# Kernel tuning notes

Measured on AMD Instinct MI355X. Metric: run time of the kernel, lower is better.

Reference implementation:

```python
import jax, jax.numpy as jnp
import numpy as np
from jax import lax

V, D, H, C = 32000, 300, 300, 3
B, T = 128, 512


def setup_inputs() -> dict:
    key = jax.random.key(0)
    ks = jax.random.split(key, 8)
    sentence_ids = jax.random.randint(ks[0], (B, T), 0, V, dtype=jnp.int32)
    lengths = jnp.maximum(jax.random.randint(ks[1], (B,), 0, T, dtype=jnp.int32), 1)
    labels = jax.random.randint(ks[2], (B,), 0, C, dtype=jnp.int32)
    embedding = jax.random.normal(ks[3], (V, D), jnp.float32) * 0.1
    W_lstm = jax.random.normal(ks[4], (D + H, 4 * H), jnp.float32) * 0.05
    b_lstm = jnp.zeros((4 * H,), jnp.float32)
    W_dense = jax.random.normal(ks[5], (H, C), jnp.float32) * 0.05
    b_dense = jnp.zeros((C,), jnp.float32)
    return {"sentence_ids": sentence_ids, "lengths": lengths, "labels": labels,
            "embedding": embedding, "W_lstm": W_lstm, "b_lstm": b_lstm,
            "W_dense": W_dense, "b_dense": b_dense}


def reference(sentence_ids, lengths, labels, embedding, W_lstm, b_lstm, W_dense, b_dense):
    # Embedding lookup: [B, T, D]
    x = embedding[sentence_ids]
    b, t, d = x.shape
    h_units = W_dense.shape[0]
    FORGET_BIAS = 1.0  # TF BasicLSTMCell default

    xs = jnp.swapaxes(x, 0, 1)                                   # [T, B, D]
    step_mask = (jnp.arange(t)[:, None] < lengths[None, :])      # [T, B]

    def step(carry, inp):
        h, c = carry
        xt, m = inp                                              # [B,D], [B]
        z = jnp.concatenate([xt, h], axis=-1) @ W_lstm + b_lstm  # [B, 4H]
        i, j, f, o = jnp.split(z, 4, axis=-1)
        new_c = c * jax.nn.sigmoid(f + FORGET_BIAS) + jax.nn.sigmoid(i) * jnp.tanh(j)
        new_h = jnp.tanh(new_c) * jax.nn.sigmoid(o)
        mm = m[:, None]
        # dynamic_rnn: freeze state past each sequence's length
        h = jnp.where(mm, new_h, h)
        c = jnp.where(mm, new_c, c)
        return (h, c), None

    h0 = jnp.zeros((b, h_units), x.dtype)
    c0 = jnp.zeros((b, h_units), x.dtype)
    (h_final, _), _ = lax.scan(step, (h0, c0), (xs, step_mask))

    logits = h_final @ W_dense + b_dense                          # [B, C]
    logp = jax.nn.log_softmax(logits, axis=-1)
    nll = -jnp.take_along_axis(logp, labels[:, None].astype(jnp.int32), axis=1)[:, 0]
    loss = jnp.mean(nll)
    return loss, logits
```

## Files before the change

kernel.cpp:

```cpp
#include <hip/hip_runtime.h>
#include <hip/hip_bf16.h>
#include <math.h>

#define VV   32000
#define DD   300
#define HU   300
#define NC   3
#define BB   128
#define TT   512
#define N4H  1200
#define CHUNK 64
#define NCHUNK (TT / CHUNK)

#define GC   15
#define GR   16
#define RPW  8
#define UPW  20
#define KSW  96
#define HLB_STRIDE 312
#define HLB_SIZE   (16 * HLB_STRIDE + 32)

static constexpr size_t ZX_F   = (size_t)BB * CHUNK * N4H;
static constexpr size_t EX_W   = (size_t)2 * GR * RPW * HU;
static constexpr size_t CST_F  = (size_t)BB * HU;
static constexpr size_t HFIN_F = (size_t)BB * HU;

typedef __attribute__((ext_vector_type(8))) short bf16x8;
typedef __attribute__((ext_vector_type(8))) _Float16 f16x8;
typedef __attribute__((ext_vector_type(4))) float f32x4;
typedef unsigned long long ull;

__device__ __forceinline__ short f2bf(float f) {
    unsigned u = __float_as_uint(f);
    u += 0x7fff + ((u >> 16) & 1);
    return (short)(u >> 16);
}
__device__ __forceinline__ short f2h(float f) {
    _Float16 h = (_Float16)f;
    return *(short*)&h;
}
__device__ __forceinline__ float h2f(short s) {
    _Float16 h = *(_Float16*)&s;
    return (float)h;
}
__device__ __forceinline__ float sigm(float x) { return 1.f / (1.f + __expf(-x)); }
__device__ __forceinline__ float tanh_(float x) { return 1.f - 2.f / (__expf(2.f * x) + 1.f); }

__global__ void init_kernel(ull* __restrict__ ex, float* __restrict__ cst,
                            float* __restrict__ out) {
    size_t i = (size_t)blockIdx.x * 256 + threadIdx.x;
    if (i < EX_W) ex[i] = 0ull;
    if (i < CST_F) cst[i] = 0.f;
    if (i == 0) out[0] = 0.f;
}

__global__ __launch_bounds__(256) void zx_gemm(
    const float* __restrict__ emb, const int* __restrict__ ids,
    const float* __restrict__ Wl, const float* __restrict__ bl,
    float* __restrict__ zx, int t0)
{
    __shared__ short A_l[256 * 40];
    __shared__ short B_l[80 * 40];
    __shared__ int   ids_l[256];

    const int tid = threadIdx.x;
    const int m0  = blockIdx.x * 256;
    const int n0  = blockIdx.y * 80;
    const int wv  = tid >> 6, ln = tid & 63;

    {
        int m = m0 + tid;
        int b = m >> 6, tc = m & (CHUNK - 1);
        ids_l[tid] = ids[b * TT + t0 + tc];
    }

    f32x4 acc[4][5];
    for (int i = 0; i < 4; ++i)
        for (int j = 0; j < 5; ++j)
            acc[i][j] = (f32x4){0.f, 0.f, 0.f, 0.f};

    for (int k0 = 0; k0 < 320; k0 += 32) {
        __syncthreads();
        {
            const float* src = emb + (size_t)ids_l[tid] * DD;
            #pragma unroll
            for (int q = 0; q < 8; ++q) {
                int kg = k0 + q * 4;
                float4 v;
                if (kg < DD) v = *(const float4*)(src + kg);
                else         v = make_float4(0.f, 0.f, 0.f, 0.f);
                short4 s; s.x = f2bf(v.x); s.y = f2bf(v.y); s.z = f2bf(v.z); s.w = f2bf(v.w);
                *(short4*)&A_l[tid * 40 + q * 4] = s;
            }
        }
        {
            int kk = tid >> 3;
            int c0 = (tid & 7) * 10;
            int kg = k0 + kk;
            #pragma unroll
            for (int c = 0; c < 10; ++c) {
                float v = (kg < DD) ? Wl[(size_t)kg * N4H + n0 + c0 + c] : 0.f;
                B_l[(c0 + c) * 40 + kk] = f2bf(v);
            }
        }
        __syncthreads();
        const int koff = (ln >> 4) * 8;
        bf16x8 afr[4], bfr[5];
        #pragma unroll
        for (int mt = 0; mt < 4; ++mt) {
            int row = wv * 64 + mt * 16 + (ln & 15);
            afr[mt] = *(const bf16x8*)&A_l[row * 40 + koff];
        }
        #pragma unroll
        for (int nt = 0; nt < 5; ++nt) {
            int col = nt * 16 + (ln & 15);
            bfr[nt] = *(const bf16x8*)&B_l[col * 40 + koff];
        }
        #pragma unroll
        for (int mt = 0; mt < 4; ++mt)
            #pragma unroll
            for (int nt = 0; nt < 5; ++nt)
                acc[mt][nt] = __builtin_amdgcn_mfma_f32_16x16x32_bf16(
                    afr[mt], bfr[nt], acc[mt][nt], 0, 0, 0);
    }
    #pragma unroll
    for (int mt = 0; mt < 4; ++mt) {
        #pragma unroll
        for (int nt = 0; nt < 5; ++nt) {
            #pragma unroll
            for (int rg = 0; rg < 4; ++rg) {
                int row = m0 + wv * 64 + mt * 16 + (ln >> 4) * 4 + rg;
                int col = n0 + nt * 16 + (ln & 15);
                zx[(size_t)row * N4H + col] = acc[mt][nt][rg] + bl[col];
            }
        }
    }
}

__global__ __launch_bounds__(256, 1) void lstm_rec(
    const float* __restrict__ zx, const float* __restrict__ Wl,
    const int* __restrict__ lens, ull* __restrict__ ex,
    float* __restrict__ cst, float* __restrict__ hfin, int t0)
{
    const int tid = threadIdx.x;
    const int wv  = tid >> 6, ln = tid & 63;
    const int rg  = blockIdx.x % GR;
    const int cgi = blockIdx.x / GR;
    const int r0  = rg * RPW;
    const int u0  = cgi * UPW;
    const int m   = ln & 15;
    const int quad = ln >> 4;

    const int pstart_tbl[4] = {0, 4, 9, 14};
    const int np_tbl[4]     = {5, 6, 6, 1};
    const int pstart = pstart_tbl[wv];
    const int np     = np_tbl[wv];

    __shared__ short h_hi[HLB_SIZE];
    __shared__ short h_lo[HLB_SIZE];
    __shared__ float zp[2][4][RPW][84];
    __shared__ short w_l[4 * 15 * 64 * 8];

    #pragma unroll
    for (int s = 0; s < 3; ++s) {
        #pragma unroll
        for (int nt = 0; nt < 5; ++nt) {
            int c    = nt * 16 + m;
            int gate = c / 20;
            int wcol = 300 * gate + u0 + (c % 20);
            f16x8 b;
            #pragma unroll
            for (int j = 0; j < 8; ++j) {
                int k = KSW * wv + 32 * s + quad * 8 + j;
                float v = (k < HU) ? Wl[(size_t)(DD + k) * N4H + wcol] : 0.f;
                b[j] = (_Float16)v;
            }
            *(f16x8*)&w_l[(((wv * 15) + (s * 5 + nt)) * 64 + ln) * 8] = b;
        }
    }
    const int nks = (wv == 3) ? 1 : 3;

    for (int i = tid; i < HLB_SIZE; i += 256) { h_hi[i] = 0; h_lo[i] = 0; }

    const int g_u = tid % UPW, g_r = tid / UPW;
    const bool gl = (tid < RPW * UPW);
    float c_reg = 0.f, ho_reg = 0.f;
    int mylen = 0;
    if (gl) {
        c_reg = cst[(size_t)(r0 + g_r) * HU + u0 + g_u];
        mylen = lens[r0 + g_r];
        if (t0 > 0) {
            ull v = __hip_atomic_load(
                ex + (((size_t)(t0 & 1) * GR + rg) * RPW + g_r) * HU + u0 + g_u,
                __ATOMIC_RELAXED, __HIP_MEMORY_SCOPE_AGENT);
            ho_reg = __uint_as_float((unsigned)v);
        }
    }
    __syncthreads();

    for (int tc = 0; tc < CHUNK; ++tc) {
        const int t = t0 + tc;
        const int par = t & 1;

        float z_pre[4];
        if (gl) {
            const float* zrow = zx + ((size_t)(r0 + g_r) * CHUNK + tc) * N4H;
            #pragma unroll
            for (int gg = 0; gg < 4; ++gg)
                z_pre[gg] = zrow[300 * gg + u0 + g_u];
        }

        if (t > 0) {
            const ull* exb = ex + ((size_t)par * GR + rg) * (RPW * HU);

            if (ln < np) {
                const ull* sp = exb + (pstart + ln) * UPW;
                while ((int)(__hip_atomic_load(sp, __ATOMIC_RELAXED,
                             __HIP_MEMORY_SCOPE_AGENT) >> 32) < t)
                    __builtin_amdgcn_s_sleep(1);
            }

            if (wv < 3) {
                unsigned pend = 0xFFFu;
                do {
                    ull v[12];
                    #pragma unroll
                    for (int k = 0; k < 12; ++k)
                        if ((pend >> k) & 1) {
                            int i = ln + (k << 6);
                            int r = i / 96, u = KSW * wv + (i % 96);
                            v[k] = __hip_atomic_load(exb + r * HU + u,
                                                     __ATOMIC_RELAXED,
                                                     __HIP_MEMORY_SCOPE_AGENT);
                        }
                    unsigned got = 0;
                    #pragma unroll
                    for (int k = 0; k < 12; ++k) {
                        if (((pend >> k) & 1) && (int)(v[k] >> 32) >= t) {
                            int i = ln + (k << 6);
                            int r = i / 96, u = KSW * wv + (i % 96);
                            int idx = r * HLB_STRIDE + u;
                            float f = __uint_as_float((unsigned)v[k]);
                            short hi = f2h(f);
                            h_hi[idx] = hi;
                            h_lo[idx] = f2h(f - h2f(hi));
                            got |= 1u << k;
                        }
                    }
                    pend &= ~got;
                    if (pend) __builtin_amdgcn_s_sleep(1);
                } while (pend);
            } else {
                unsigned pend = (ln < 32) ? 0x3u : 0x1u;
                do {
                    ull v[2];
                    #pragma unroll
                    for (int k = 0; k < 2; ++k)
                        if ((pend >> k) & 1) {
                            int i = ln + (k << 6);
                            int r = i / 12, u = 288 + (i % 12);
                            v[k] = __hip_atomic_load(exb + r * HU + u,
                                                     __ATOMIC_RELAXED,
                                                     __HIP_MEMORY_SCOPE_AGENT);
                        }
                    unsigned got = 0;
                    #pragma unroll
                    for (int k = 0; k < 2; ++k) {
                        if (((pend >> k) & 1) && (int)(v[k] >> 32) >= t) {
                            int i = ln + (k << 6);
                            int r = i / 12, u = 288 + (i % 12);
                            int idx = r * HLB_STRIDE + u;
                            float f = __uint_as_float((unsigned)v[k]);
                            short hi = f2h(f);
                            h_hi[idx] = hi;
                            h_lo[idx] = f2h(f - h2f(hi));
                            got |= 1u << k;
                        }
                    }
                    pend &= ~got;
                    if (pend) __builtin_amdgcn_s_sleep(1);
                } while (pend);
            }
        }

        f32x4 acc[5];
        #pragma unroll
        for (int nt = 0; nt < 5; ++nt) acc[nt] = (f32x4){0.f, 0.f, 0.f, 0.f};
        for (int s = 0; s < nks; ++s) {
            const int aoff = m * HLB_STRIDE + KSW * wv + 32 * s + quad * 8;
            f16x8 ah = *(const f16x8*)&h_hi[aoff];
            f16x8 al = *(const f16x8*)&h_lo[aoff];
            f16x8 bfr[5];
            #pragma unroll
            for (int nt = 0; nt < 5; ++nt)
                bfr[nt] = *(const f16x8*)&w_l[(((wv * 15) + (s * 5 + nt)) * 64 + ln) * 8];
            #pragma unroll
            for (int nt = 0; nt < 5; ++nt)
                acc[nt] = __builtin_amdgcn_mfma_f32_16x16x32_f16(
                    ah, bfr[nt], acc[nt], 0, 0, 0);
            #pragma unroll
            for (int nt = 0; nt < 5; ++nt)
                acc[nt] = __builtin_amdgcn_mfma_f32_16x16x32_f16(
                    al, bfr[nt], acc[nt], 0, 0, 0);
        }
        if (ln < 32) {
            #pragma unroll
            for (int nt = 0; nt < 5; ++nt)
                #pragma unroll
                for (int r4 = 0; r4 < 4; ++r4)
                    zp[par][wv][quad * 4 + r4][nt * 16 + m] = acc[nt][r4];
        }
        __syncthreads();

        if (gl) {
            const int b = r0 + g_r;
            float z4[4];
            #pragma unroll
            for (int gg = 0; gg < 4; ++gg) {
                int cidx = gg * UPW + g_u;
                z4[gg] = z_pre[gg] + zp[par][0][g_r][cidx] + zp[par][1][g_r][cidx]
                                   + zp[par][2][g_r][cidx] + zp[par][3][g_r][cidx];
            }
            float ig = sigm(z4[0]);
            float jg = tanh_(z4[1]);
            float fg = sigm(z4[2] + 1.0f);
            float og = sigm(z4[3]);
            float c_new = c_reg * fg + ig * jg;
            float h_new = tanh_(c_new) * og;
            bool upd = (t < mylen);
            ho_reg = upd ? h_new : ho_reg;
            c_reg  = upd ? c_new : c_reg;
            ull pk = ((ull)(unsigned)(t + 1) << 32) | (ull)__float_as_uint(ho_reg);
            __hip_atomic_store(
                ex + (((size_t)((t + 1) & 1) * GR + rg) * RPW + g_r) * HU + u0 + g_u,
                pk, __ATOMIC_RELAXED, __HIP_MEMORY_SCOPE_AGENT);
            if (tc == CHUNK - 1) hfin[(size_t)b * HU + u0 + g_u] = ho_reg;
        }
    }
    if (gl) cst[(size_t)(r0 + g_r) * HU + u0 + g_u] = c_reg;
}

__global__ __launch_bounds__(64) void cls_kernel(
    const float* __restrict__ hfin, const float* __restrict__ Wd,
    const float* __restrict__ bd, const int* __restrict__ labels,
    float* __restrict__ out)
{
    const int b = blockIdx.x;
    const int ln = threadIdx.x;
    const float* h = hfin + (size_t)b * HU;
    float p0 = 0.f, p1 = 0.f, p2 = 0.f;
    for (int k = ln; k < HU; k += 64) {
        float hv = h[k];
        p0 += hv * Wd[k * 3 + 0];
        p1 += hv * Wd[k * 3 + 1];
        p2 += hv * Wd[k * 3 + 2];
    }
    #pragma unroll
    for (int off = 32; off > 0; off >>= 1) {
        p0 += __shfl_down(p0, off);
        p1 += __shfl_down(p1, off);
        p2 += __shfl_down(p2, off);
    }
    if (ln == 0) {
        float l0 = p0 + bd[0], l1 = p1 + bd[1], l2 = p2 + bd[2];
        float m = fmaxf(l0, fmaxf(l1, l2));
        float lse = m + logf(__expf(l0 - m) + __expf(l1 - m) + __expf(l2 - m));
        int lab = labels[b];
        float sel = (lab == 0) ? l0 : ((lab == 1) ? l1 : l2);
        float nll = lse - sel;
        out[1 + b * 3 + 0] = l0;
        out[1 + b * 3 + 1] = l1;
        out[1 + b * 3 + 2] = l2;
        atomicAdd(out, nll * (1.0f / BB));
    }
}

extern "C" void kernel_launch(void* const* d_in, const int* in_sizes, int n_in,
                              void* d_out, int out_size, void* d_ws, size_t ws_size,
                              hipStream_t stream) {
    const int*   ids  = (const int*)d_in[0];
    const int*   lens = (const int*)d_in[1];
    const int*   labs = (const int*)d_in[2];
    const float* emb  = (const float*)d_in[3];
    const float* Wl   = (const float*)d_in[4];
    const float* bl   = (const float*)d_in[5];
    const float* Wd   = (const float*)d_in[6];
    const float* bd   = (const float*)d_in[7];
    float* out = (float*)d_out;

    float* zx   = (float*)d_ws;
    ull*   ex   = (ull*)(zx + ZX_F);
    float* cst  = (float*)(ex + EX_W);
    float* hfin = cst + CST_F;

    {
        int n = (int)((EX_W + 255) / 256);
        init_kernel<<<n, 256, 0, stream>>>(ex, cst, out);
    }
    for (int c = 0; c < NCHUNK; ++c) {
        int t0 = c * CHUNK;
        zx_gemm<<<dim3(32, 15), 256, 0, stream>>>(emb, ids, Wl, bl, zx, t0);
        lstm_rec<<<GR * GC, 256, 0, stream>>>(zx, Wl, lens, ex, cst, hfin, t0);
    }
    cls_kernel<<<BB, 64, 0, stream>>>(hfin, Wd, bd, labs, out);
}
```

Before: 2.312 ms.

## Fuse input projection GEMM into recurrent LSTM kernel per timestep

Removes the separate zx_gemm kernel and its global zx buffer. Inside the recurrent kernel each wave now gathers the embedding rows for its batch rows at each timestep, converts them to bf16, and runs an extra bf16 MFMA against an input-weight slice kept in shared memory, adding the result into the same accumulator as the hidden-state product. The intent is to drop the global write and read of the precomputed gate inputs and the per-chunk kernel launches. In exchange every step adds embedding gather latency and more MFMAs to the serial critical path, and the double-buffered zp array is replaced by a single buffer guarded by an extra barrier per step.

```diff
diff --git a/kernel.cpp b/kernel.cpp
--- a/kernel.cpp
+++ b/kernel.cpp
@@ -20,7 +20,6 @@
 #define HLB_STRIDE 312
 #define HLB_SIZE   (16 * HLB_STRIDE + 32)
 
-static constexpr size_t ZX_F   = (size_t)BB * CHUNK * N4H;
 static constexpr size_t EX_W   = (size_t)2 * GR * RPW * HU;
 static constexpr size_t CST_F  = (size_t)BB * HU;
 static constexpr size_t HFIN_F = (size_t)BB * HU;
@@ -54,91 +53,9 @@
     if (i == 0) out[0] = 0.f;
 }
 
-__global__ __launch_bounds__(256) void zx_gemm(
+__global__ __launch_bounds__(256, 1) void lstm_rec(
     const float* __restrict__ emb, const int* __restrict__ ids,
     const float* __restrict__ Wl, const float* __restrict__ bl,
-    float* __restrict__ zx, int t0)
-{
-    __shared__ short A_l[256 * 40];
-    __shared__ short B_l[80 * 40];
-    __shared__ int   ids_l[256];
-
-    const int tid = threadIdx.x;
-    const int m0  = blockIdx.x * 256;
-    const int n0  = blockIdx.y * 80;
-    const int wv  = tid >> 6, ln = tid & 63;
-
-    {
-        int m = m0 + tid;
-        int b = m >> 6, tc = m & (CHUNK - 1);
-        ids_l[tid] = ids[b * TT + t0 + tc];
-    }
-
-    f32x4 acc[4][5];
-    for (int i = 0; i < 4; ++i)
-        for (int j = 0; j < 5; ++j)
-            acc[i][j] = (f32x4){0.f, 0.f, 0.f, 0.f};
-
-    for (int k0 = 0; k0 < 320; k0 += 32) {
-        __syncthreads();
-        {
-            const float* src = emb + (size_t)ids_l[tid] * DD;
-            #pragma unroll
-            for (int q = 0; q < 8; ++q) {
-                int kg = k0 + q * 4;
-                float4 v;
-                if (kg < DD) v = *(const float4*)(src + kg);
-                else         v = make_float4(0.f, 0.f, 0.f, 0.f);
-                short4 s; s.x = f2bf(v.x); s.y = f2bf(v.y); s.z = f2bf(v.z); s.w = f2bf(v.w);
-                *(short4*)&A_l[tid * 40 + q * 4] = s;
-            }
-        }
-        {
-            int kk = tid >> 3;
-            int c0 = (tid & 7) * 10;
-            int kg = k0 + kk;
-            #pragma unroll
-            for (int c = 0; c < 10; ++c) {
-                float v = (kg < DD) ? Wl[(size_t)kg * N4H + n0 + c0 + c] : 0.f;
-                B_l[(c0 + c) * 40 + kk] = f2bf(v);
-            }
-        }
-        __syncthreads();
-        const int koff = (ln >> 4) * 8;
-        bf16x8 afr[4], bfr[5];
-        #pragma unroll
-        for (int mt = 0; mt < 4; ++mt) {
-            int row = wv * 64 + mt * 16 + (ln & 15);
-            afr[mt] = *(const bf16x8*)&A_l[row * 40 + koff];
-        }
-        #pragma unroll
-        for (int nt = 0; nt < 5; ++nt) {
-            int col = nt * 16 + (ln & 15);
-            bfr[nt] = *(const bf16x8*)&B_l[col * 40 + koff];
-        }
-        #pragma unroll
-        for (int mt = 0; mt < 4; ++mt)
-            #pragma unroll
-            for (int nt = 0; nt < 5; ++nt)
-                acc[mt][nt] = __builtin_amdgcn_mfma_f32_16x16x32_bf16(
-                    afr[mt], bfr[nt], acc[mt][nt], 0, 0, 0);
-    }
-    #pragma unroll
-    for (int mt = 0; mt < 4; ++mt) {
-        #pragma unroll
-        for (int nt = 0; nt < 5; ++nt) {
-            #pragma unroll
-            for (int rg = 0; rg < 4; ++rg) {
-                int row = m0 + wv * 64 + mt * 16 + (ln >> 4) * 4 + rg;
-                int col = n0 + nt * 16 + (ln & 15);
-                zx[(size_t)row * N4H + col] = acc[mt][nt][rg] + bl[col];
-            }
-        }
-    }
-}
-
-__global__ __launch_bounds__(256, 1) void lstm_rec(
-    const float* __restrict__ zx, const float* __restrict__ Wl,
     const int* __restrict__ lens, ull* __restrict__ ex,
     float* __restrict__ cst, float* __restrict__ hfin, int t0)
 {
@@ -158,8 +75,10 @@
 
     __shared__ short h_hi[HLB_SIZE];
     __shared__ short h_lo[HLB_SIZE];
-    __shared__ float zp[2][4][RPW][84];
+    __shared__ float zp[4][RPW][84];
     __shared__ short w_l[4 * 15 * 64 * 8];
+    __shared__ short w_lx[4 * 15 * 64 * 8];
+    __shared__ int   ids_l[RPW][CHUNK];
 
     #pragma unroll
     for (int s = 0; s < 3; ++s) {
@@ -168,27 +87,40 @@
             int c    = nt * 16 + m;
             int gate = c / 20;
             int wcol = 300 * gate + u0 + (c % 20);
-            f16x8 b;
+            f16x8 bh;
+            bf16x8 bx;
             #pragma unroll
             for (int j = 0; j < 8; ++j) {
                 int k = KSW * wv + 32 * s + quad * 8 + j;
-                float v = (k < HU) ? Wl[(size_t)(DD + k) * N4H + wcol] : 0.f;
-                b[j] = (_Float16)v;
-            }
-            *(f16x8*)&w_l[(((wv * 15) + (s * 5 + nt)) * 64 + ln) * 8] = b;
+                float vh = (k < HU) ? Wl[(size_t)(DD + k) * N4H + wcol] : 0.f;
+                float vx = (k < DD) ? Wl[(size_t)k * N4H + wcol] : 0.f;
+                bh[j] = (_Float16)vh;
+                bx[j] = f2bf(vx);
+            }
+            int fo = (((wv * 15) + (s * 5 + nt)) * 64 + ln) * 8;
+            *(f16x8*)&w_l[fo]  = bh;
+            *(bf16x8*)&w_lx[fo] = bx;
         }
     }
     const int nks = (wv == 3) ? 1 : 3;
 
     for (int i = tid; i < HLB_SIZE; i += 256) { h_hi[i] = 0; h_lo[i] = 0; }
+
+    for (int i = tid; i < RPW * CHUNK; i += 256) {
+        int r = i >> 6, tcc = i & 63;
+        ids_l[r][tcc] = ids[(size_t)(r0 + r) * TT + t0 + tcc];
+    }
 
     const int g_u = tid % UPW, g_r = tid / UPW;
     const bool gl = (tid < RPW * UPW);
     float c_reg = 0.f, ho_reg = 0.f;
+    float blr[4] = {0.f, 0.f, 0.f, 0.f};
     int mylen = 0;
     if (gl) {
         c_reg = cst[(size_t)(r0 + g_r) * HU + u0 + g_u];
         mylen = lens[r0 + g_r];
+        #pragma unroll
+        for (int gg = 0; gg < 4; ++gg) blr[gg] = bl[300 * gg + u0 + g_u];
         if (t0 > 0) {
             ull v = __hip_atomic_load(
                 ex + (((size_t)(t0 & 1) * GR + rg) * RPW + g_r) * HU + u0 + g_u,
@@ -202,12 +134,32 @@
         const int t = t0 + tc;
         const int par = t & 1;
 
-        float z_pre[4];
-        if (gl) {
-            const float* zrow = zx + ((size_t)(r0 + g_r) * CHUNK + tc) * N4H;
-            #pragma unroll
-            for (int gg = 0; gg < 4; ++gg)
-                z_pre[gg] = zrow[300 * gg + u0 + g_u];
+        bf16x8 xa[3];
+        #pragma unroll
+        for (int s = 0; s < 3; ++s)
+            #pragma unroll
+            for (int j = 0; j < 8; ++j) xa[s][j] = 0;
+        if (m < RPW) {
+            const float* xrow = emb + (size_t)ids_l[m][tc] * DD;
+            if (wv < 3) {
+                #pragma unroll
+                for (int s = 0; s < 3; ++s) {
+                    int kb = KSW * wv + 32 * s + quad * 8;
+                    float4 p = *(const float4*)(xrow + kb);
+                    float4 q = *(const float4*)(xrow + kb + 4);
+                    xa[s][0] = f2bf(p.x); xa[s][1] = f2bf(p.y);
+                    xa[s][2] = f2bf(p.z); xa[s][3] = f2bf(p.w);
+                    xa[s][4] = f2bf(q.x); xa[s][5] = f2bf(q.y);
+                    xa[s][6] = f2bf(q.z); xa[s][7] = f2bf(q.w);
+                }
+            } else {
+                int kb = KSW * 3 + quad * 8;
+                #pragma unroll
+                for (int j = 0; j < 8; ++j) {
+                    int k = kb + j;
+                    xa[0][j] = (k < DD) ? f2bf(xrow[k]) : (short)0;
+                }
+            }
         }
 
         if (t > 0) {
@@ -290,25 +242,25 @@
             const int aoff = m * HLB_STRIDE + KSW * wv + 32 * s + quad * 8;
             f16x8 ah = *(const f16x8*)&h_hi[aoff];
             f16x8 al = *(const f16x8*)&h_lo[aoff];
-            f16x8 bfr[5];
-            #pragma unroll
-            for (int nt = 0; nt < 5; ++nt)
-                bfr[nt] = *(const f16x8*)&w_l[(((wv * 15) + (s * 5 + nt)) * 64 + ln) * 8];
-            #pragma unroll
-            for (int nt = 0; nt < 5; ++nt)
+            #pragma unroll
+            for (int nt = 0; nt < 5; ++nt) {
+                int fo = (((wv * 15) + (s * 5 + nt)) * 64 + ln) * 8;
+                f16x8  bh = *(const f16x8*)&w_l[fo];
+                bf16x8 bx = *(const bf16x8*)&w_lx[fo];
                 acc[nt] = __builtin_amdgcn_mfma_f32_16x16x32_f16(
-                    ah, bfr[nt], acc[nt], 0, 0, 0);
-            #pragma unroll
-            for (int nt = 0; nt < 5; ++nt)
+                    ah, bh, acc[nt], 0, 0, 0);
                 acc[nt] = __builtin_amdgcn_mfma_f32_16x16x32_f16(
-                    al, bfr[nt], acc[nt], 0, 0, 0);
+                    al, bh, acc[nt], 0, 0, 0);
+                acc[nt] = __builtin_amdgcn_mfma_f32_16x16x32_bf16(
+                    xa[s], bx, acc[nt], 0, 0, 0);
+            }
         }
         if (ln < 32) {
             #pragma unroll
             for (int nt = 0; nt < 5; ++nt)
                 #pragma unroll
                 for (int r4 = 0; r4 < 4; ++r4)
-                    zp[par][wv][quad * 4 + r4][nt * 16 + m] = acc[nt][r4];
+                    zp[wv][quad * 4 + r4][nt * 16 + m] = acc[nt][r4];
         }
         __syncthreads();
 
@@ -318,8 +270,8 @@
             #pragma unroll
             for (int gg = 0; gg < 4; ++gg) {
                 int cidx = gg * UPW + g_u;
-                z4[gg] = z_pre[gg] + zp[par][0][g_r][cidx] + zp[par][1][g_r][cidx]
-                                   + zp[par][2][g_r][cidx] + zp[par][3][g_r][cidx];
+                z4[gg] = blr[gg] + zp[0][g_r][cidx] + zp[1][g_r][cidx]
+                                 + zp[2][g_r][cidx] + zp[3][g_r][cidx];
             }
             float ig = sigm(z4[0]);
             float jg = tanh_(z4[1]);
@@ -336,6 +288,7 @@
                 pk, __ATOMIC_RELAXED, __HIP_MEMORY_SCOPE_AGENT);
             if (tc == CHUNK - 1) hfin[(size_t)b * HU + u0 + g_u] = ho_reg;
         }
+        __syncthreads();
     }
     if (gl) cst[(size_t)(r0 + g_r) * HU + u0 + g_u] = c_reg;
 }
@@ -388,8 +341,7 @@
     const float* bd   = (const float*)d_in[7];
     float* out = (float*)d_out;
 
-    float* zx   = (float*)d_ws;
-    ull*   ex   = (ull*)(zx + ZX_F);
+    ull*   ex   = (ull*)d_ws;
     float* cst  = (float*)(ex + EX_W);
     float* hfin = cst + CST_F;
 
@@ -399,8 +351,8 @@
     }
     for (int c = 0; c < NCHUNK; ++c) {
         int t0 = c * CHUNK;
-        zx_gemm<<<dim3(32, 15), 256, 0, stream>>>(emb, ids, Wl, bl, zx, t0);
-        lstm_rec<<<GR * GC, 256, 0, stream>>>(zx, Wl, lens, ex, cst, hfin, t0);
+        lstm_rec<<<GR * GC, 256, 0, stream>>>(emb, ids, Wl, bl, lens,
+                                              ex, cst, hfin, t0);
     }
     cls_kernel<<<BB, 64, 0, stream>>>(hfin, Wd, bd, labs, out);
 }
```

New measurement: 3.714 ms. 60.7% more time.
